# Optimization experiments

Hardware: AMD Instinct MI355X
Metric: run time of the kernel (lower is better)

The kernel has to match this reference:

```python
import jax, jax.numpy as jnp
import numpy as np

# dims matching init_kwargs / input_specs
N, C, H, W = 8, 256, 64, 64
OUT_C, KH, KW = 256, 3, 3
STRIDE, PAD = 1, 1
OUT_H = (H - KH + 2 * PAD) // STRIDE + 1  # 64
OUT_W = (W - KW + 2 * PAD) // STRIDE + 1  # 64
K = KH * KW


def setup_inputs() -> dict:
    key = jax.random.key(0)
    k1, k2, k3 = jax.random.split(key, 3)
    x = jax.random.normal(k1, (N, C, H, W), dtype=jnp.float32)
    offset = jax.random.normal(k2, (N, 2 * K, OUT_H, OUT_W), dtype=jnp.float32)
    # kaiming-uniform-ish scale for weight (fan_in = C*KH*KW)
    bound = 1.0 / np.sqrt(C * KH * KW)
    weight = jax.random.uniform(k3, (OUT_C, C, KH, KW), dtype=jnp.float32,
                                minval=-bound, maxval=bound)
    return {"input": x, "offset": offset, "weight": weight}


def _deform_conv(x, offset, weight):
    # base sampling positions in pixel coords: y = oy*stride + ky - pad
    ky = jnp.repeat(jnp.arange(KH, dtype=jnp.float32) - PAD, KW)  # [K]
    kx = jnp.tile(jnp.arange(KW, dtype=jnp.float32) - PAD, KH)    # [K]
    oy = jnp.arange(OUT_H, dtype=jnp.float32) * STRIDE            # [outH]
    ox = jnp.arange(OUT_W, dtype=jnp.float32) * STRIDE            # [outW]
    base_y = ky[:, None, None] + oy[None, :, None]  # [K, outH, 1]
    base_x = kx[:, None, None] + ox[None, None, :]  # [K, 1, outW]

    off = offset.reshape(N, K, 2, OUT_H, OUT_W)
    y = base_y[None] + off[:, :, 0]  # [N, K, outH, outW], offset channel 0 = dy
    xp = base_x[None] + off[:, :, 1]  # channel 1 = dx

    # bilinear sample with zero padding (grid_sample align_corners=True, zeros)
    y0 = jnp.floor(y)
    x0 = jnp.floor(xp)
    bidx = jnp.arange(N)[:, None, None, None]
    acc = jnp.zeros((N, K, OUT_H, OUT_W, C), dtype=x.dtype)
    for dy in (0.0, 1.0):
        for dx in (0.0, 1.0):
            yi = y0 + dy
            xi = x0 + dx
            wgt = (1.0 - jnp.abs(y - yi)) * (1.0 - jnp.abs(xp - xi))
            valid = ((yi >= 0) & (yi <= H - 1) & (xi >= 0) & (xi <= W - 1))
            yc = jnp.clip(yi, 0, H - 1).astype(jnp.int32)
            xc = jnp.clip(xi, 0, W - 1).astype(jnp.int32)
            g = x[bidx, :, yc, xc]  # [N, K, outH, outW, C]
            acc = acc + g * (wgt * valid.astype(x.dtype))[..., None]

    # weight.view(outC, -1) flattens (C, KH, KW) -> (C, K) ordering
    w = weight.reshape(OUT_C, C, K)
    out = jnp.einsum('nkhwc,ock->nohw', acc, w)  # [N, outC, outH, outW]
    return out


def reference(input, offset, weight):
    # NOTE: original forward never adds bias -> faithfully omitted
    return _deform_conv(input, offset, weight)
```

## Files before the change

### kernel.cpp

```cpp
#include <hip/hip_runtime.h>
#include <hip/hip_fp16.h>
#include <stdint.h>


typedef _Float16 half8 __attribute__((ext_vector_type(8)));
typedef float f32x4 __attribute__((ext_vector_type(4)));

__device__ __forceinline__ __half2 h2(uint32_t u) {
  return __builtin_bit_cast(__half2, u);
}
__device__ __forceinline__ uint32_t packh2f(float a, float b) {
  return __builtin_bit_cast(uint32_t, __floats2half2_rn(a, b));
}
__device__ __forceinline__ __half2 duplo(uint32_t u) {
  return __half2half2(__builtin_bit_cast(__half, (unsigned short)(u & 0xffffu)));
}
__device__ __forceinline__ __half2 duphi(uint32_t u) {
  return __half2half2(__builtin_bit_cast(__half, (unsigned short)(u >> 16)));
}

__global__ __launch_bounds__(256) void prep_all_kernel(
    const float* __restrict__ x, const float* __restrict__ w,
    const float* __restrict__ offset,
    unsigned short* __restrict__ xb, unsigned short* __restrict__ w3s,
    unsigned short* __restrict__ coords) {
  __shared__ float tile[64][65];
  int tid = threadIdx.x;
  if (blockIdx.x < 2048) {
    int bn   = blockIdx.x >> 8;
    int rem  = blockIdx.x & 255;
    int y    = rem >> 2;
    int cblk = rem & 3;
    const float* src = x + ((size_t)(bn * 256 + cblk * 64)) * 4096 + y * 64;
#pragma unroll
    for (int i = 0; i < 4; ++i) {
      int u  = i * 256 + tid;
      int cl = u >> 4;
      int xs = (u & 15) * 4;
      float4 v = *(const float4*)(src + cl * 4096 + xs);
      tile[cl][xs] = v.x; tile[cl][xs + 1] = v.y;
      tile[cl][xs + 2] = v.z; tile[cl][xs + 3] = v.w;
    }
    __syncthreads();
    unsigned short* dst = xb + ((size_t)(bn * 64 + y) * 64) * 256 + cblk * 64;
#pragma unroll
    for (int i = 0; i < 8; ++i) {
      int v2  = i * 256 + tid;
      int xc  = v2 >> 5;
      int cl2 = (v2 & 31) * 2;
      *(uint32_t*)(dst + xc * 256 + cl2) = packh2f(tile[cl2][xc], tile[cl2 + 1][xc]);
    }
  } else if (blockIdx.x < 4352) {
    int idx = (blockIdx.x - 2048) * 256 + tid;
    int t    = idx >> 14;
    int r2   = idx & 16383;
    int e    = r2 & 7;
    int lane = (r2 >> 3) & 63;
    int ks   = (r2 >> 9) & 1;
    int nn   = (r2 >> 10) & 3;
    int wcol = (r2 >> 12) & 3;
    int oc = wcol * 64 + nn * 16 + (lane & 15);
    int kk = (ks * 4 + (lane >> 4)) * 8 + e;
    int c  = (t & 3) * 64 + kk;
    int k  = t >> 2;
    w3s[idx] = __builtin_bit_cast(unsigned short, __float2half(w[(oc * 256 + c) * 9 + k]));
  } else {
    int idx = (blockIdx.x - 4352) * 256 + tid;
    int ow  = idx & 63;
    int oh  = (idx >> 6) & 63;
    int r   = idx >> 12;
    int k   = r % 9;
    int bn  = r / 9;
    int ky = k / 3 - 1;
    int kx = k % 3 - 1;
    float offy = offset[((bn * 18 + 2 * k    ) * 64 + oh) * 64 + ow];
    float offx = offset[((bn * 18 + 2 * k + 1) * 64 + oh) * 64 + ow];
    float y = (float)(oh + ky) + offy;
    float x2 = (float)(ow + kx) + offx;
    float y0f = floorf(y), x0f = floorf(x2);
    float fy = y - y0f, fx = x2 - x0f;
    int y0 = (int)y0f, x0 = (int)x0f;
    int y1 = y0 + 1, x1 = x0 + 1;
    float vy0 = (y0 >= 0 && y0 <= 63) ? 1.0f : 0.0f;
    float vy1 = (y1 >= 0 && y1 <= 63) ? 1.0f : 0.0f;
    float vx0 = (x0 >= 0 && x0 <= 63) ? 1.0f : 0.0f;
    float vx1 = (x1 >= 0 && x1 <= 63) ? 1.0f : 0.0f;
    float wy0 = (1.0f - fy) * vy0, wy1 = fy * vy1;
    float wx0 = (1.0f - fx) * vx0, wx1 = fx * vx1;
    int y0c = min(max(y0, 0), 63), y1c = min(max(y1, 0), 63);
    int x0c = min(max(x0, 0), 63), x1c = min(max(x1, 0), 63);
    unsigned short ent[8];
    ent[0] = __builtin_bit_cast(unsigned short, __float2half(wy0 * wx0));
    ent[1] = __builtin_bit_cast(unsigned short, __float2half(wy0 * wx1));
    ent[2] = __builtin_bit_cast(unsigned short, __float2half(wy1 * wx0));
    ent[3] = __builtin_bit_cast(unsigned short, __float2half(wy1 * wx1));
    ent[4] = (unsigned short)(y0c * 64 + x0c);
    ent[5] = (unsigned short)(y0c * 64 + x1c);
    ent[6] = (unsigned short)(y1c * 64 + x0c);
    ent[7] = (unsigned short)(y1c * 64 + x1c);
    *(uint4*)(coords + (size_t)idx * 8) = *(const uint4*)ent;
  }
}

__global__ __launch_bounds__(512, 2) void deform_mfma_kernel(
    const unsigned short* __restrict__ xb,
    const unsigned short* __restrict__ coords,
    const unsigned short* __restrict__ w3s,
    float* __restrict__ out) {
  __shared__ __align__(16) unsigned short At[2][64 * 64];

  int bn  = blockIdx.x & 7;
  int oh  = blockIdx.x >> 3;
  int tid = threadIdx.x;

  int w    = tid >> 6;
  int lane = tid & 63;
  int wrow = w & 1;
  int wcol = w >> 1;
  int mrow = lane & 15;
  int quad = lane >> 4;

  int srow = tid >> 3;
  int sg   = tid & 7;

  const char* xbc = (const char*)(xb + (size_t)bn * (64 * 64 * 256));
  const unsigned short* cb = coords + ((size_t)((bn * 9) * 64 + oh) * 64 + srow) * 8;

  int aw0  = srow * 64 + ((sg ^ (srow & 7)) * 8);
  int grp0 = quad ^ (mrow & 7);
  int grp1 = (4 + quad) ^ (mrow & 7);
  int a_base = (wrow * 32 + mrow) * 64;
  int b_off  = wcol * 8192 + lane * 16;

  f32x4 acc[2][4] = {};
  half8 bC[2][4];

  __half2 w00, w01, w02, w03;
  uint32_t o00, o01, o02, o03;
  uint4 cn, gc0, gc1, gc2, gc3;

#define BLOADR(TT, BS)                                                          \
  {                                                                             \
    const char* wp = (const char*)w3s + (size_t)(TT) * 32768 + b_off;           \
    _Pragma("unroll")                                                           \
    for (int nn = 0; nn < 4; ++nn) {                                            \
      BS[0][nn] = *(const half8*)(wp + (nn * 2 + 0) * 1024);                    \
      BS[1][nn] = *(const half8*)(wp + (nn * 2 + 1) * 1024);                    \
    }                                                                           \
  }

#define TAPSETUP_R(CE)                                                          \
  {                                                                             \
    w00 = duplo((CE).x); w01 = duphi((CE).x);                                   \
    w02 = duplo((CE).y); w03 = duphi((CE).y);                                   \
    o00 = (((CE).z & 0xffffu) << 9) + sg * 16;                                  \
    o01 = (((CE).z >> 16) << 9) + sg * 16;                                      \
    o02 = (((CE).w & 0xffffu) << 9) + sg * 16;                                  \
    o03 = (((CE).w >> 16) << 9) + sg * 16;                                      \
  }

#define AGATHER(TT)                                                             \
  {                                                                             \
    gc0 = *(const uint4*)(xbc + o00 + ((TT) & 3) * 128);                        \
    gc1 = *(const uint4*)(xbc + o01 + ((TT) & 3) * 128);                        \
    gc2 = *(const uint4*)(xbc + o02 + ((TT) & 3) * 128);                        \
    gc3 = *(const uint4*)(xbc + o03 + ((TT) & 3) * 128);                        \
  }

#define AMATH(ATP)                                                              \
  {                                                                             \
    __half2 r0 = __hmul2(h2(gc0.x), w00);                                       \
    r0 = __hfma2(h2(gc1.x), w01, r0); r0 = __hfma2(h2(gc2.x), w02, r0);         \
    r0 = __hfma2(h2(gc3.x), w03, r0);                                           \
    __half2 r1 = __hmul2(h2(gc0.y), w00);                                       \
    r1 = __hfma2(h2(gc1.y), w01, r1); r1 = __hfma2(h2(gc2.y), w02, r1);         \
    r1 = __hfma2(h2(gc3.y), w03, r1);                                           \
    __half2 r2 = __hmul2(h2(gc0.z), w00);                                       \
    r2 = __hfma2(h2(gc1.z), w01, r2); r2 = __hfma2(h2(gc2.z), w02, r2);         \
    r2 = __hfma2(h2(gc3.z), w03, r2);                                           \
    __half2 r3 = __hmul2(h2(gc0.w), w00);                                       \
    r3 = __hfma2(h2(gc1.w), w01, r3); r3 = __hfma2(h2(gc2.w), w02, r3);         \
    r3 = __hfma2(h2(gc3.w), w03, r3);                                           \
    uint4 pk;                                                                   \
    pk.x = __builtin_bit_cast(uint32_t, r0);                                    \
    pk.y = __builtin_bit_cast(uint32_t, r1);                                    \
    pk.z = __builtin_bit_cast(uint32_t, r2);                                    \
    pk.w = __builtin_bit_cast(uint32_t, r3);                                    \
    *(uint4*)((ATP) + aw0) = pk;                                                \
  }

#define COMPUTE(ATP, BS)                                                        \
  {                                                                             \
    _Pragma("unroll")                                                           \
    for (int m = 0; m < 2; ++m) {                                               \
      half8 af0 = *(const half8*)((ATP) + a_base + m * 1024 + grp0 * 8);        \
      half8 af1 = *(const half8*)((ATP) + a_base + m * 1024 + grp1 * 8);        \
      _Pragma("unroll")                                                         \
      for (int nn = 0; nn < 4; ++nn) {                                          \
        acc[m][nn] = __builtin_amdgcn_mfma_f32_16x16x32_f16(af0, BS[0][nn], acc[m][nn], 0, 0, 0); \
        acc[m][nn] = __builtin_amdgcn_mfma_f32_16x16x32_f16(af1, BS[1][nn], acc[m][nn], 0, 0, 0); \
      }                                                                         \
    }                                                                           \
  }

  {
    uint4 ce0 = *(const uint4*)cb;
    TAPSETUP_R(ce0)
  }
  AGATHER(0)
  AMATH(&At[0][0])
  __syncthreads();

  for (int tap = 0; tap < 9; ++tap) {
#pragma unroll
    for (int cc = 0; cc < 4; ++cc) {
      const int t = tap * 4 + cc;
      BLOADR(t, bC)
      if (t < 35) {
        if (cc == 2 && tap < 8) cn = *(const uint4*)(cb + (tap + 1) * 32768);
        if (cc == 3) TAPSETUP_R(cn)
        AGATHER(t + 1)
      }
      if (cc & 1) { COMPUTE(&At[1][0], bC) } else { COMPUTE(&At[0][0], bC) }
      if (t < 35) {
        if (cc & 1) { AMATH(&At[0][0]) } else { AMATH(&At[1][0]) }
      }
      __syncthreads();
    }
  }

  float* outp = out + (size_t)bn * 256 * 4096 + (size_t)oh * 64;
#pragma unroll
  for (int m = 0; m < 2; ++m) {
    int ow0 = wrow * 32 + m * 16 + quad * 4;
#pragma unroll
    for (int nn = 0; nn < 4; ++nn) {
      int oc = wcol * 64 + nn * 16 + mrow;
      *(f32x4*)(outp + (size_t)oc * 4096 + ow0) = acc[m][nn];
    }
  }
#undef BLOADR
#undef TAPSETUP_R
#undef AGATHER
#undef AMATH
#undef COMPUTE
}

extern "C" void kernel_launch(void* const* d_in, const int* in_sizes, int n_in,
                              void* d_out, int out_size, void* d_ws, size_t ws_size,
                              hipStream_t stream) {
  (void)in_sizes; (void)n_in; (void)out_size; (void)ws_size;
  const float* x      = (const float*)d_in[0];
  const float* offset = (const float*)d_in[1];
  const float* weight = (const float*)d_in[2];
  float* out = (float*)d_out;

  unsigned short* xb     = (unsigned short*)d_ws;
  unsigned short* w3s    = xb + (size_t)8 * 64 * 64 * 256;
  unsigned short* coords = w3s + (size_t)36 * 16384;

  prep_all_kernel<<<5504, 256, 0, stream>>>(x, weight, offset, xb, w3s, coords);
  deform_mfma_kernel<<<512, 512, 0, stream>>>(xb, coords, w3s, out);
}
```

Baseline: 155.1 us.

## Halve block tile to 32 columns, double-buffer B fragments, use lightweight barrier

Each block now covers half an output row (32 columns) with 256 threads, and the grid doubles to 1024 blocks to raise occupancy and improve load balance across CUs. The weight (B) fragments are double-buffered in registers and prefetched one step ahead so global loads overlap the MFMA work. The __syncthreads is replaced by an LDS-only waitcnt plus s_barrier, and MFMA sections are wrapped in s_setprio. The trade-off is that each block reloads the full weight slice for half the output, doubling B traffic per output, and the extra B buffer raises register pressure.

```diff
diff --git a/kernel.cpp b/kernel.cpp
--- a/kernel.cpp
+++ b/kernel.cpp
@@ -102,21 +102,21 @@
   }
 }
 
-__global__ __launch_bounds__(512, 2) void deform_mfma_kernel(
+__global__ __launch_bounds__(256, 3) void deform_mfma_kernel(
     const unsigned short* __restrict__ xb,
     const unsigned short* __restrict__ coords,
     const unsigned short* __restrict__ w3s,
     float* __restrict__ out) {
-  __shared__ __align__(16) unsigned short At[2][64 * 64];
+  __shared__ __align__(16) unsigned short At[2][32 * 64];
 
   int bn  = blockIdx.x & 7;
-  int oh  = blockIdx.x >> 3;
-  int tid = threadIdx.x;
-
-  int w    = tid >> 6;
+  int rem = blockIdx.x >> 3;
+  int oh  = rem >> 1;
+  int owh = rem & 1;
+
+  int tid  = threadIdx.x;
+  int wcol = tid >> 6;
   int lane = tid & 63;
-  int wrow = w & 1;
-  int wcol = w >> 1;
   int mrow = lane & 15;
   int quad = lane >> 4;
 
@@ -124,20 +124,28 @@
   int sg   = tid & 7;
 
   const char* xbc = (const char*)(xb + (size_t)bn * (64 * 64 * 256));
-  const unsigned short* cb = coords + ((size_t)((bn * 9) * 64 + oh) * 64 + srow) * 8;
+  const unsigned short* cb =
+      coords + ((size_t)((bn * 9) * 64 + oh) * 64 + owh * 32 + srow) * 8;
 
   int aw0  = srow * 64 + ((sg ^ (srow & 7)) * 8);
   int grp0 = quad ^ (mrow & 7);
   int grp1 = (4 + quad) ^ (mrow & 7);
-  int a_base = (wrow * 32 + mrow) * 64;
+  int a_base = mrow * 64;
   int b_off  = wcol * 8192 + lane * 16;
 
   f32x4 acc[2][4] = {};
-  half8 bC[2][4];
+  half8 bA[2][4], bB[2][4];
 
   __half2 w00, w01, w02, w03;
   uint32_t o00, o01, o02, o03;
   uint4 cn, gc0, gc1, gc2, gc3;
+
+#define CBAR()                                                                  \
+  {                                                                             \
+    asm volatile("s_waitcnt lgkmcnt(0)" ::: "memory");                          \
+    __builtin_amdgcn_s_barrier();                                               \
+    asm volatile("" ::: "memory");                                              \
+  }
 
 #define BLOADR(TT, BS)                                                          \
   {                                                                             \
@@ -191,54 +199,59 @@
 
 #define COMPUTE(ATP, BS)                                                        \
   {                                                                             \
+    half8 af00 = *(const half8*)((ATP) + a_base + grp0 * 8);                    \
+    half8 af01 = *(const half8*)((ATP) + a_base + grp1 * 8);                    \
+    half8 af10 = *(const half8*)((ATP) + a_base + 1024 + grp0 * 8);             \
+    half8 af11 = *(const half8*)((ATP) + a_base + 1024 + grp1 * 8);             \
+    __builtin_amdgcn_s_setprio(1);                                              \
     _Pragma("unroll")                                                           \
-    for (int m = 0; m < 2; ++m) {                                               \
-      half8 af0 = *(const half8*)((ATP) + a_base + m * 1024 + grp0 * 8);        \
-      half8 af1 = *(const half8*)((ATP) + a_base + m * 1024 + grp1 * 8);        \
-      _Pragma("unroll")                                                         \
-      for (int nn = 0; nn < 4; ++nn) {                                          \
-        acc[m][nn] = __builtin_amdgcn_mfma_f32_16x16x32_f16(af0, BS[0][nn], acc[m][nn], 0, 0, 0); \
-        acc[m][nn] = __builtin_amdgcn_mfma_f32_16x16x32_f16(af1, BS[1][nn], acc[m][nn], 0, 0, 0); \
-      }                                                                         \
+    for (int nn = 0; nn < 4; ++nn) {                                            \
+      acc[0][nn] = __builtin_amdgcn_mfma_f32_16x16x32_f16(af00, BS[0][nn], acc[0][nn], 0, 0, 0); \
+      acc[0][nn] = __builtin_amdgcn_mfma_f32_16x16x32_f16(af01, BS[1][nn], acc[0][nn], 0, 0, 0); \
+      acc[1][nn] = __builtin_amdgcn_mfma_f32_16x16x32_f16(af10, BS[0][nn], acc[1][nn], 0, 0, 0); \
+      acc[1][nn] = __builtin_amdgcn_mfma_f32_16x16x32_f16(af11, BS[1][nn], acc[1][nn], 0, 0, 0); \
     }                                                                           \
+    __builtin_amdgcn_s_setprio(0);                                              \
   }
 
   {
     uint4 ce0 = *(const uint4*)cb;
     TAPSETUP_R(ce0)
   }
+  BLOADR(0, bA)
   AGATHER(0)
   AMATH(&At[0][0])
-  __syncthreads();
+  CBAR()
 
   for (int tap = 0; tap < 9; ++tap) {
 #pragma unroll
     for (int cc = 0; cc < 4; ++cc) {
       const int t = tap * 4 + cc;
-      BLOADR(t, bC)
       if (t < 35) {
+        if (cc & 1) { BLOADR(t + 1, bA) } else { BLOADR(t + 1, bB) }
         if (cc == 2 && tap < 8) cn = *(const uint4*)(cb + (tap + 1) * 32768);
         if (cc == 3) TAPSETUP_R(cn)
         AGATHER(t + 1)
       }
-      if (cc & 1) { COMPUTE(&At[1][0], bC) } else { COMPUTE(&At[0][0], bC) }
+      if (cc & 1) { COMPUTE(&At[1][0], bB) } else { COMPUTE(&At[0][0], bA) }
       if (t < 35) {
         if (cc & 1) { AMATH(&At[0][0]) } else { AMATH(&At[1][0]) }
+        CBAR()
       }
-      __syncthreads();
-    }
-  }
-
-  float* outp = out + (size_t)bn * 256 * 4096 + (size_t)oh * 64;
+    }
+  }
+
+  float* outp = out + (size_t)bn * 256 * 4096 + (size_t)oh * 64 + owh * 32;
 #pragma unroll
   for (int m = 0; m < 2; ++m) {
-    int ow0 = wrow * 32 + m * 16 + quad * 4;
+    int ow0 = m * 16 + quad * 4;
 #pragma unroll
     for (int nn = 0; nn < 4; ++nn) {
       int oc = wcol * 64 + nn * 16 + mrow;
       *(f32x4*)(outp + (size_t)oc * 4096 + ow0) = acc[m][nn];
     }
   }
+#undef CBAR
 #undef BLOADR
 #undef TAPSETUP_R
 #undef AGATHER
@@ -260,5 +273,5 @@
   unsigned short* coords = w3s + (size_t)36 * 16384;
 
   prep_all_kernel<<<5504, 256, 0, stream>>>(x, weight, offset, xb, w3s, coords);
-  deform_mfma_kernel<<<512, 512, 0, stream>>>(xb, coords, w3s, out);
-}
+  deform_mfma_kernel<<<1024, 256, 0, stream>>>(xb, coords, w3s, out);
+}
```

Result: faster. 150.7 us (-2.8%).

## Process two output rows per block to reuse weight fragments across 128-pixel tile

Applied to the files above, without the earlier changes.

Each block now computes two output rows (a 128x256 tile) instead of one, so every weight B-fragment loaded from global memory feeds twice as many MFMAs. The grid is halved to 256 blocks, and the LDS A-buffer, gather registers and accumulators all double. Weight loads are double-buffered one step ahead. The barrier becomes a custom lgkmcnt wait plus s_barrier, and MFMA sections get raised wave priority. In exchange, register pressure and per-block LDS go up, and only 256 blocks may underfill the GPU's compute units, reducing parallelism.

```diff
diff --git a/kernel.cpp b/kernel.cpp
--- a/kernel.cpp
+++ b/kernel.cpp
@@ -107,10 +107,10 @@
     const unsigned short* __restrict__ coords,
     const unsigned short* __restrict__ w3s,
     float* __restrict__ out) {
-  __shared__ __align__(16) unsigned short At[2][64 * 64];
+  __shared__ __align__(16) unsigned short At[2][128 * 64];
 
   int bn  = blockIdx.x & 7;
-  int oh  = blockIdx.x >> 3;
+  int ohp = blockIdx.x >> 3;
   int tid = threadIdx.x;
 
   int w    = tid >> 6;
@@ -124,20 +124,29 @@
   int sg   = tid & 7;
 
   const char* xbc = (const char*)(xb + (size_t)bn * (64 * 64 * 256));
-  const unsigned short* cb = coords + ((size_t)((bn * 9) * 64 + oh) * 64 + srow) * 8;
+  const unsigned short* cb0 = coords + ((size_t)((bn * 9) * 64 + ohp * 2) * 64 + srow) * 8;
+  const unsigned short* cb1 = cb0 + 512;
 
   int aw0  = srow * 64 + ((sg ^ (srow & 7)) * 8);
   int grp0 = quad ^ (mrow & 7);
   int grp1 = (4 + quad) ^ (mrow & 7);
-  int a_base = (wrow * 32 + mrow) * 64;
+  int a_base = (wrow * 64 + mrow) * 64;
   int b_off  = wcol * 8192 + lane * 16;
 
-  f32x4 acc[2][4] = {};
-  half8 bC[2][4];
-
-  __half2 w00, w01, w02, w03;
-  uint32_t o00, o01, o02, o03;
-  uint4 cn, gc0, gc1, gc2, gc3;
+  f32x4 acc[4][4] = {};
+  half8 bA[2][4], bB[2][4];
+
+  __half2 w00, w01, w02, w03, w10, w11, w12, w13;
+  uint32_t o00, o01, o02, o03, o10, o11, o12, o13;
+  uint4 cn0, cn1;
+  uint4 ga0, ga1, ga2, ga3, gb0, gb1, gb2, gb3;
+
+#define CBAR()                                                                  \
+  {                                                                             \
+    asm volatile("s_waitcnt lgkmcnt(0)" ::: "memory");                          \
+    __builtin_amdgcn_s_barrier();                                               \
+    asm volatile("" ::: "memory");                                              \
+  }
 
 #define BLOADR(TT, BS)                                                          \
   {                                                                             \
@@ -149,50 +158,79 @@
     }                                                                           \
   }
 
-#define TAPSETUP_R(CE)                                                          \
-  {                                                                             \
-    w00 = duplo((CE).x); w01 = duphi((CE).x);                                   \
-    w02 = duplo((CE).y); w03 = duphi((CE).y);                                   \
-    o00 = (((CE).z & 0xffffu) << 9) + sg * 16;                                  \
-    o01 = (((CE).z >> 16) << 9) + sg * 16;                                      \
-    o02 = (((CE).w & 0xffffu) << 9) + sg * 16;                                  \
-    o03 = (((CE).w >> 16) << 9) + sg * 16;                                      \
+#define TAPSETUP_R(CE0, CE1)                                                    \
+  {                                                                             \
+    w00 = duplo((CE0).x); w01 = duphi((CE0).x);                                 \
+    w02 = duplo((CE0).y); w03 = duphi((CE0).y);                                 \
+    o00 = (((CE0).z & 0xffffu) << 9) + sg * 16;                                 \
+    o01 = (((CE0).z >> 16) << 9) + sg * 16;                                     \
+    o02 = (((CE0).w & 0xffffu) << 9) + sg * 16;                                 \
+    o03 = (((CE0).w >> 16) << 9) + sg * 16;                                     \
+    w10 = duplo((CE1).x); w11 = duphi((CE1).x);                                 \
+    w12 = duplo((CE1).y); w13 = duphi((CE1).y);                                 \
+    o10 = (((CE1).z & 0xffffu) << 9) + sg * 16;                                 \
+    o11 = (((CE1).z >> 16) << 9) + sg * 16;                                     \
+    o12 = (((CE1).w & 0xffffu) << 9) + sg * 16;                                 \
+    o13 = (((CE1).w >> 16) << 9) + sg * 16;                                     \
   }
 
 #define AGATHER(TT)                                                             \
   {                                                                             \
-    gc0 = *(const uint4*)(xbc + o00 + ((TT) & 3) * 128);                        \
-    gc1 = *(const uint4*)(xbc + o01 + ((TT) & 3) * 128);                        \
-    gc2 = *(const uint4*)(xbc + o02 + ((TT) & 3) * 128);                        \
-    gc3 = *(const uint4*)(xbc + o03 + ((TT) & 3) * 128);                        \
+    ga0 = *(const uint4*)(xbc + o00 + ((TT) & 3) * 128);                        \
+    ga1 = *(const uint4*)(xbc + o01 + ((TT) & 3) * 128);                        \
+    ga2 = *(const uint4*)(xbc + o02 + ((TT) & 3) * 128);                        \
+    ga3 = *(const uint4*)(xbc + o03 + ((TT) & 3) * 128);                        \
+    gb0 = *(const uint4*)(xbc + o10 + ((TT) & 3) * 128);                        \
+    gb1 = *(const uint4*)(xbc + o11 + ((TT) & 3) * 128);                        \
+    gb2 = *(const uint4*)(xbc + o12 + ((TT) & 3) * 128);                        \
+    gb3 = *(const uint4*)(xbc + o13 + ((TT) & 3) * 128);                        \
   }
 
 #define AMATH(ATP)                                                              \
   {                                                                             \
-    __half2 r0 = __hmul2(h2(gc0.x), w00);                                       \
-    r0 = __hfma2(h2(gc1.x), w01, r0); r0 = __hfma2(h2(gc2.x), w02, r0);         \
-    r0 = __hfma2(h2(gc3.x), w03, r0);                                           \
-    __half2 r1 = __hmul2(h2(gc0.y), w00);                                       \
-    r1 = __hfma2(h2(gc1.y), w01, r1); r1 = __hfma2(h2(gc2.y), w02, r1);         \
-    r1 = __hfma2(h2(gc3.y), w03, r1);                                           \
-    __half2 r2 = __hmul2(h2(gc0.z), w00);                                       \
-    r2 = __hfma2(h2(gc1.z), w01, r2); r2 = __hfma2(h2(gc2.z), w02, r2);         \
-    r2 = __hfma2(h2(gc3.z), w03, r2);                                           \
-    __half2 r3 = __hmul2(h2(gc0.w), w00);                                       \
-    r3 = __hfma2(h2(gc1.w), w01, r3); r3 = __hfma2(h2(gc2.w), w02, r3);         \
-    r3 = __hfma2(h2(gc3.w), w03, r3);                                           \
+    __half2 r0 = __hmul2(h2(ga0.x), w00);                                       \
+    r0 = __hfma2(h2(ga1.x), w01, r0); r0 = __hfma2(h2(ga2.x), w02, r0);         \
+    r0 = __hfma2(h2(ga3.x), w03, r0);                                           \
+    __half2 r1 = __hmul2(h2(ga0.y), w00);                                       \
+    r1 = __hfma2(h2(ga1.y), w01, r1); r1 = __hfma2(h2(ga2.y), w02, r1);         \
+    r1 = __hfma2(h2(ga3.y), w03, r1);                                           \
+    __half2 r2 = __hmul2(h2(ga0.z), w00);                                       \
+    r2 = __hfma2(h2(ga1.z), w01, r2); r2 = __hfma2(h2(ga2.z), w02, r2);         \
+    r2 = __hfma2(h2(ga3.z), w03, r2);                                           \
+    __half2 r3 = __hmul2(h2(ga0.w), w00);                                       \
+    r3 = __hfma2(h2(ga1.w), w01, r3); r3 = __hfma2(h2(ga2.w), w02, r3);         \
+    r3 = __hfma2(h2(ga3.w), w03, r3);                                           \
     uint4 pk;                                                                   \
     pk.x = __builtin_bit_cast(uint32_t, r0);                                    \
     pk.y = __builtin_bit_cast(uint32_t, r1);                                    \
     pk.z = __builtin_bit_cast(uint32_t, r2);                                    \
     pk.w = __builtin_bit_cast(uint32_t, r3);                                    \
     *(uint4*)((ATP) + aw0) = pk;                                                \
+    __half2 s0 = __hmul2(h2(gb0.x), w10);                                       \
+    s0 = __hfma2(h2(gb1.x), w11, s0); s0 = __hfma2(h2(gb2.x), w12, s0);         \
+    s0 = __hfma2(h2(gb3.x), w13, s0);                                           \
+    __half2 s1 = __hmul2(h2(gb0.y), w10);                                       \
+    s1 = __hfma2(h2(gb1.y), w11, s1); s1 = __hfma2(h2(gb2.y), w12, s1);         \
+    s1 = __hfma2(h2(gb3.y), w13, s1);                                           \
+    __half2 s2 = __hmul2(h2(gb0.z), w10);                                       \
+    s2 = __hfma2(h2(gb1.z), w11, s2); s2 = __hfma2(h2(gb2.z), w12, s2);         \
+    s2 = __hfma2(h2(gb3.z), w13, s2);                                           \
+    __half2 s3 = __hmul2(h2(gb0.w), w10);                                       \
+    s3 = __hfma2(h2(gb1.w), w11, s3); s3 = __hfma2(h2(gb2.w), w12, s3);         \
+    s3 = __hfma2(h2(gb3.w), w13, s3);                                           \
+    uint4 qk;                                                                   \
+    qk.x = __builtin_bit_cast(uint32_t, s0);                                    \
+    qk.y = __builtin_bit_cast(uint32_t, s1);                                    \
+    qk.z = __builtin_bit_cast(uint32_t, s2);                                    \
+    qk.w = __builtin_bit_cast(uint32_t, s3);                                    \
+    *(uint4*)((ATP) + aw0 + 4096) = qk;                                         \
   }
 
 #define COMPUTE(ATP, BS)                                                        \
   {                                                                             \
+    __builtin_amdgcn_s_setprio(1);                                              \
     _Pragma("unroll")                                                           \
-    for (int m = 0; m < 2; ++m) {                                               \
+    for (int m = 0; m < 4; ++m) {                                               \
       half8 af0 = *(const half8*)((ATP) + a_base + m * 1024 + grp0 * 8);        \
       half8 af1 = *(const half8*)((ATP) + a_base + m * 1024 + grp1 * 8);        \
       _Pragma("unroll")                                                         \
@@ -201,44 +239,51 @@
         acc[m][nn] = __builtin_amdgcn_mfma_f32_16x16x32_f16(af1, BS[1][nn], acc[m][nn], 0, 0, 0); \
       }                                                                         \
     }                                                                           \
+    __builtin_amdgcn_s_setprio(0);                                              \
   }
 
   {
-    uint4 ce0 = *(const uint4*)cb;
-    TAPSETUP_R(ce0)
+    uint4 ce0 = *(const uint4*)cb0;
+    uint4 ce1 = *(const uint4*)cb1;
+    TAPSETUP_R(ce0, ce1)
   }
   AGATHER(0)
+  BLOADR(0, bA)
   AMATH(&At[0][0])
-  __syncthreads();
+  CBAR()
 
   for (int tap = 0; tap < 9; ++tap) {
 #pragma unroll
     for (int cc = 0; cc < 4; ++cc) {
       const int t = tap * 4 + cc;
-      BLOADR(t, bC)
       if (t < 35) {
-        if (cc == 2 && tap < 8) cn = *(const uint4*)(cb + (tap + 1) * 32768);
-        if (cc == 3) TAPSETUP_R(cn)
+        if (cc == 3) TAPSETUP_R(cn0, cn1)
         AGATHER(t + 1)
+        if (cc == 2 && tap < 8) {
+          cn0 = *(const uint4*)(cb0 + (tap + 1) * 32768);
+          cn1 = *(const uint4*)(cb1 + (tap + 1) * 32768);
+        }
+        if (cc & 1) { BLOADR(t + 1, bA) } else { BLOADR(t + 1, bB) }
       }
-      if (cc & 1) { COMPUTE(&At[1][0], bC) } else { COMPUTE(&At[0][0], bC) }
+      if (cc & 1) { COMPUTE(&At[1][0], bB) } else { COMPUTE(&At[0][0], bA) }
       if (t < 35) {
         if (cc & 1) { AMATH(&At[0][0]) } else { AMATH(&At[1][0]) }
       }
-      __syncthreads();
+      CBAR()
     }
   }
 
-  float* outp = out + (size_t)bn * 256 * 4096 + (size_t)oh * 64;
-#pragma unroll
-  for (int m = 0; m < 2; ++m) {
-    int ow0 = wrow * 32 + m * 16 + quad * 4;
+  float* outp = out + (size_t)bn * 256 * 4096 + (size_t)(ohp * 2 + wrow) * 64;
+#pragma unroll
+  for (int m = 0; m < 4; ++m) {
+    int ow0 = m * 16 + quad * 4;
 #pragma unroll
     for (int nn = 0; nn < 4; ++nn) {
       int oc = wcol * 64 + nn * 16 + mrow;
       *(f32x4*)(outp + (size_t)oc * 4096 + ow0) = acc[m][nn];
     }
   }
+#undef CBAR
 #undef BLOADR
 #undef TAPSETUP_R
 #undef AGATHER
@@ -260,5 +305,5 @@
   unsigned short* coords = w3s + (size_t)36 * 16384;
 
   prep_all_kernel<<<5504, 256, 0, stream>>>(x, weight, offset, xb, w3s, coords);
-  deform_mfma_kernel<<<512, 512, 0, stream>>>(xb, coords, w3s, out);
-}
+  deform_mfma_kernel<<<256, 512, 0, stream>>>(xb, coords, w3s, out);
+}
```

After: 140.7 us. 9.2% less time.
